# Kernel optimization log

Hardware: AMD Instinct MI355X
Metric: run time of the kernel (lower is better)

## Reference

```python
import jax, jax.numpy as jnp
import numpy as np

B, T, C, N = 2, 2048, 4096, 4096

def setup_inputs() -> dict:
    key = jax.random.key(0)
    k1, k2, k3, k4 = jax.random.split(key, 4)
    y = jax.random.normal(k1, (B, T, C), dtype=jnp.float32)
    # quantized weight: uint8 codes in [0,255], stored/used as float after upcast
    weight = jnp.round(jax.random.uniform(k2, (C, N), dtype=jnp.float32) * 255.0)
    rng = jax.random.uniform(k3, (1, 1, C), dtype=jnp.float32) * 0.01  # per-input-channel scale
    offset = jax.random.normal(k4, (C,), dtype=jnp.float32) * 0.01    # per-input-channel offset
    return {"y": y, "weight": weight, "rng": rng, "offset": offset}

def reference(y, weight, rng, offset):
    # yv = y.reshape(-1,C) @ offset -> [B,T,1] correction term
    yv = jnp.einsum('btc,c->bt', y, offset)[..., None]
    # (y * range) @ weight  (dequantized GEMM) + correction
    out = jnp.einsum('btc,cn->btn', y * rng, weight) + yv
    return out
```

## Files before the change

kernel.cpp:

```cpp
#include <hip/hip_runtime.h>

typedef unsigned short u16;
typedef unsigned int u32;
typedef unsigned char u8;
typedef signed char i8;

typedef int i32x4 __attribute__((ext_vector_type(4)));

__global__ __launch_bounds__(256) void quant_y_kernel(const float* __restrict__ y,
                                                      const float* __restrict__ rng,
                                                      const float* __restrict__ off,
                                                      uint4* __restrict__ qy,
                                                      float* __restrict__ sp,
                                                      float* __restrict__ tv) {
    const int row = blockIdx.x;
    const int tid = threadIdx.x;
    const float* yr = y + (size_t)row * 4096;
    const int base = tid * 16;

    float ysr[16];
    float amax = 0.0f, s1 = 0.0f, s2 = 0.0f;
    #pragma unroll
    for (int ii = 0; ii < 4; ++ii) {
        float4 v = *(const float4*)&yr[base + ii * 4];
        float4 g = *(const float4*)&rng[base + ii * 4];
        float4 o = *(const float4*)&off[base + ii * 4];
        float p0 = v.x * g.x, p1 = v.y * g.y, p2 = v.z * g.z, p3 = v.w * g.w;
        ysr[ii * 4 + 0] = p0; ysr[ii * 4 + 1] = p1;
        ysr[ii * 4 + 2] = p2; ysr[ii * 4 + 3] = p3;
        s1 += p0 + p1 + p2 + p3;
        s2 += v.x * o.x + v.y * o.y + v.z * o.z + v.w * o.w;
        amax = fmaxf(amax, fmaxf(fmaxf(fabsf(p0), fabsf(p1)), fmaxf(fabsf(p2), fabsf(p3))));
    }
    #pragma unroll
    for (int d = 32; d > 0; d >>= 1) {
        amax = fmaxf(amax, __shfl_down(amax, d));
        s1 += __shfl_down(s1, d);
        s2 += __shfl_down(s2, d);
    }
    __shared__ float ra[4], rs1[4], rs2[4];
    const int wv = tid >> 6;
    if ((tid & 63) == 0) { ra[wv] = amax; rs1[wv] = s1; rs2[wv] = s2; }
    __syncthreads();
    const float sm = fmaxf(fmaxf(ra[0], ra[1]), fmaxf(ra[2], ra[3]));
    const float inv = sm > 0.0f ? 127.0f / sm : 0.0f;

    u32 d[4];
    #pragma unroll
    for (int g = 0; g < 4; ++g) {
        u32 b0 = (u8)(i8)(int)rintf(ysr[g * 4 + 0] * inv);
        u32 b1 = (u8)(i8)(int)rintf(ysr[g * 4 + 1] * inv);
        u32 b2 = (u8)(i8)(int)rintf(ysr[g * 4 + 2] * inv);
        u32 b3 = (u8)(i8)(int)rintf(ysr[g * 4 + 3] * inv);
        d[g] = b0 | (b1 << 8) | (b2 << 16) | (b3 << 24);
    }
    const int j = (tid & 7) ^ (row & 7);
    qy[(size_t)row * 256 + (tid >> 3) * 8 + j] = make_uint4(d[0], d[1], d[2], d[3]);
    if (tid == 0) {
        sp[row] = sm / 127.0f;
        tv[row] = 128.0f * (rs1[0] + rs1[1] + rs1[2] + rs1[3])
                        + (rs2[0] + rs2[1] + rs2[2] + rs2[3]);
    }
}

__global__ __launch_bounds__(256) void quant_w_kernel(const float* __restrict__ w,
                                                      uint4* __restrict__ wq) {
    __shared__ i8 tile[64][68];
    const int n0 = (blockIdx.x & 63) * 64;
    const int k0 = (blockIdx.x >> 6) * 64;
    const int c4 = threadIdx.x & 15;
    const int r0 = threadIdx.x >> 4;
    #pragma unroll
    for (int i = 0; i < 4; ++i) {
        int kk = r0 + i * 16;
        float4 v = *(const float4*)&w[(size_t)(k0 + kk) * 4096 + n0 + c4 * 4];
        u32 b0 = (u8)(i8)((int)v.x - 128);
        u32 b1 = (u8)(i8)((int)v.y - 128);
        u32 b2 = (u8)(i8)((int)v.z - 128);
        u32 b3 = (u8)(i8)((int)v.w - 128);
        *(u32*)&tile[kk][c4 * 4] = b0 | (b1 << 8) | (b2 << 16) | (b3 << 24);
    }
    __syncthreads();
    const int nl = threadIdx.x >> 2;
    const int ci = threadIdx.x & 3;
    const int l = ((k0 >> 4) & 7) + ci;
    const int j = l ^ ((n0 + nl) & 7);
    u32 d[4];
    #pragma unroll
    for (int g = 0; g < 4; ++g) {
        int kl = ci * 16 + g * 4;
        d[g] = (u32)(u8)tile[kl + 0][nl] | ((u32)(u8)tile[kl + 1][nl] << 8)
             | ((u32)(u8)tile[kl + 2][nl] << 16) | ((u32)(u8)tile[kl + 3][nl] << 24);
    }
    wq[(size_t)(n0 + nl) * 256 + (k0 >> 7) * 8 + j] = make_uint4(d[0], d[1], d[2], d[3]);
}

__device__ inline void gld16(const i8* g, i8* l) {
    __builtin_amdgcn_global_load_lds((const __attribute__((address_space(1))) void*)g,
                                     (__attribute__((address_space(3))) void*)l,
                                     16, 0, 0);
}

__global__ __launch_bounds__(256) void gemm_kernel(const i8* __restrict__ qy,
                                                   const i8* __restrict__ wq,
                                                   const float* __restrict__ sp,
                                                   const float* __restrict__ tv,
                                                   float* __restrict__ out) {
    __shared__ i8 As[128 * 128];
    __shared__ i8 Bs[128 * 128];
    const int bid = blockIdx.x;
    const int xcd = bid & 7;
    const int jj = bid >> 3;
    const int bn = (xcd * 4 + (jj & 3)) * 128;
    const int bm = (jj >> 2) * 128;

    const int lane = threadIdx.x & 63;
    const int wv = threadIdx.x >> 6;
    const int wm = (wv >> 1) * 64;
    const int wn = (wv & 1) * 64;
    const int r = lane & 15;
    const int q = lane >> 4;
    const int j0 = q ^ (r & 7);

    const int rsub = lane >> 3;
    const int jsub = lane & 7;
    const i8* gA[4]; const i8* gB[4]; i8* lA[4]; i8* lB[4];
    #pragma unroll
    for (int c = 0; c < 4; ++c) {
        int ca = wv * 4 + c;
        gA[c] = qy + (size_t)(bm + ca * 8 + rsub) * 4096 + jsub * 16;
        gB[c] = wq + (size_t)(bn + ca * 8 + rsub) * 4096 + jsub * 16;
        lA[c] = &As[ca * 1024];
        lB[c] = &Bs[ca * 1024];
    }

    i32x4 acc[4][4] = {};

    for (int kt = 0; kt < 32; ++kt) {
        #pragma unroll
        for (int c = 0; c < 4; ++c) {
            gld16(gA[c], lA[c]);
            gld16(gB[c], lB[c]);
            gA[c] += 128; gB[c] += 128;
        }
        __syncthreads();

        #pragma unroll
        for (int s = 0; s < 2; ++s) {
            const int js = (j0 ^ (s * 4)) * 16;
            i32x4 af[4], bfr[4];
            #pragma unroll
            for (int i = 0; i < 4; ++i)
                af[i] = *(const i32x4*)&As[(wm + i * 16 + r) * 128 + js];
            #pragma unroll
            for (int i = 0; i < 4; ++i)
                bfr[i] = *(const i32x4*)&Bs[(wn + i * 16 + r) * 128 + js];
            #pragma unroll
            for (int i = 0; i < 4; ++i) {
                #pragma unroll
                for (int j = 0; j < 4; ++j)
                    acc[i][j] = __builtin_amdgcn_mfma_i32_16x16x64_i8(af[i], bfr[j], acc[i][j], 0, 0, 0);
            }
        }
        __syncthreads();
    }

    #pragma unroll
    for (int i = 0; i < 4; ++i) {
        #pragma unroll
        for (int rr = 0; rr < 4; ++rr) {
            const int gm = bm + wm + i * 16 + q * 4 + rr;
            const float sc = sp[gm];
            const float tt = tv[gm];
            #pragma unroll
            for (int j = 0; j < 4; ++j) {
                const int gn = bn + wn + j * 16 + r;
                out[(size_t)gm * 4096 + gn] = sc * (float)acc[i][j][rr] + tt;
            }
        }
    }
}

extern "C" void kernel_launch(void* const* d_in, const int* in_sizes, int n_in,
                              void* d_out, int out_size, void* d_ws, size_t ws_size,
                              hipStream_t stream) {
    const float* y   = (const float*)d_in[0];
    const float* w   = (const float*)d_in[1];
    const float* rng = (const float*)d_in[2];
    const float* off = (const float*)d_in[3];
    float* out = (float*)d_out;

    i8* qy = (i8*)d_ws;
    i8* wq = qy + (size_t)4096 * 4096;
    float* sp = (float*)(wq + (size_t)4096 * 4096);
    float* tv = sp + 4096;

    quant_y_kernel<<<4096, 256, 0, stream>>>(y, rng, off, (uint4*)qy, sp, tv);
    quant_w_kernel<<<4096, 256, 0, stream>>>(w, (uint4*)wq);
    gemm_kernel<<<1024, 256, 0, stream>>>(qy, wq, sp, tv, out);
}
```

Before: 244.4 us.

## Merge quantization kernels and enlarge GEMM tile to 256x128

The two quantization kernels become one launch, with block index ranges choosing between activation and weight work, which removes one kernel launch and lets the two overlap. The int8 GEMM block tile grows from 128x128 to 256x128, so each wave computes 128x64 with 32 accumulators and reuses each B fragment across eight A fragments. This halves the grid to 512 blocks and raises arithmetic intensity per LDS byte. The cost is more LDS per block (48KB) and more accumulator registers, which lowers occupancy and leaves fewer blocks to fill the CUs.

```diff
diff --git a/kernel.cpp b/kernel.cpp
--- a/kernel.cpp
+++ b/kernel.cpp
@@ -7,92 +7,92 @@
 
 typedef int i32x4 __attribute__((ext_vector_type(4)));
 
-__global__ __launch_bounds__(256) void quant_y_kernel(const float* __restrict__ y,
-                                                      const float* __restrict__ rng,
-                                                      const float* __restrict__ off,
-                                                      uint4* __restrict__ qy,
-                                                      float* __restrict__ sp,
-                                                      float* __restrict__ tv) {
-    const int row = blockIdx.x;
+__global__ __launch_bounds__(256) void prep_kernel(const float* __restrict__ y,
+                                                   const float* __restrict__ w,
+                                                   const float* __restrict__ rng,
+                                                   const float* __restrict__ off,
+                                                   uint4* __restrict__ qy,
+                                                   uint4* __restrict__ wq,
+                                                   float* __restrict__ sp,
+                                                   float* __restrict__ tv) {
     const int tid = threadIdx.x;
-    const float* yr = y + (size_t)row * 4096;
-    const int base = tid * 16;
-
-    float ysr[16];
-    float amax = 0.0f, s1 = 0.0f, s2 = 0.0f;
-    #pragma unroll
-    for (int ii = 0; ii < 4; ++ii) {
-        float4 v = *(const float4*)&yr[base + ii * 4];
-        float4 g = *(const float4*)&rng[base + ii * 4];
-        float4 o = *(const float4*)&off[base + ii * 4];
-        float p0 = v.x * g.x, p1 = v.y * g.y, p2 = v.z * g.z, p3 = v.w * g.w;
-        ysr[ii * 4 + 0] = p0; ysr[ii * 4 + 1] = p1;
-        ysr[ii * 4 + 2] = p2; ysr[ii * 4 + 3] = p3;
-        s1 += p0 + p1 + p2 + p3;
-        s2 += v.x * o.x + v.y * o.y + v.z * o.z + v.w * o.w;
-        amax = fmaxf(amax, fmaxf(fmaxf(fabsf(p0), fabsf(p1)), fmaxf(fabsf(p2), fabsf(p3))));
+    if (blockIdx.x < 4096) {
+        const int row = blockIdx.x;
+        const float* yr = y + (size_t)row * 4096;
+        const int base = tid * 16;
+        float ysr[16];
+        float amax = 0.0f, s1 = 0.0f, s2 = 0.0f;
+        #pragma unroll
+        for (int ii = 0; ii < 4; ++ii) {
+            float4 v = *(const float4*)&yr[base + ii * 4];
+            float4 g = *(const float4*)&rng[base + ii * 4];
+            float4 o = *(const float4*)&off[base + ii * 4];
+            float p0 = v.x * g.x, p1 = v.y * g.y, p2 = v.z * g.z, p3 = v.w * g.w;
+            ysr[ii * 4 + 0] = p0; ysr[ii * 4 + 1] = p1;
+            ysr[ii * 4 + 2] = p2; ysr[ii * 4 + 3] = p3;
+            s1 += p0 + p1 + p2 + p3;
+            s2 += v.x * o.x + v.y * o.y + v.z * o.z + v.w * o.w;
+            amax = fmaxf(amax, fmaxf(fmaxf(fabsf(p0), fabsf(p1)), fmaxf(fabsf(p2), fabsf(p3))));
+        }
+        #pragma unroll
+        for (int d = 32; d > 0; d >>= 1) {
+            amax = fmaxf(amax, __shfl_down(amax, d));
+            s1 += __shfl_down(s1, d);
+            s2 += __shfl_down(s2, d);
+        }
+        __shared__ float ra[4], rs1[4], rs2[4];
+        const int wv = tid >> 6;
+        if ((tid & 63) == 0) { ra[wv] = amax; rs1[wv] = s1; rs2[wv] = s2; }
+        __syncthreads();
+        const float sm = fmaxf(fmaxf(ra[0], ra[1]), fmaxf(ra[2], ra[3]));
+        const float inv = sm > 0.0f ? 127.0f / sm : 0.0f;
+        u32 d[4];
+        #pragma unroll
+        for (int g = 0; g < 4; ++g) {
+            u32 b0 = (u8)(i8)(int)rintf(ysr[g * 4 + 0] * inv);
+            u32 b1 = (u8)(i8)(int)rintf(ysr[g * 4 + 1] * inv);
+            u32 b2 = (u8)(i8)(int)rintf(ysr[g * 4 + 2] * inv);
+            u32 b3 = (u8)(i8)(int)rintf(ysr[g * 4 + 3] * inv);
+            d[g] = b0 | (b1 << 8) | (b2 << 16) | (b3 << 24);
+        }
+        const int j = (tid & 7) ^ (row & 7);
+        qy[(size_t)row * 256 + (tid >> 3) * 8 + j] = make_uint4(d[0], d[1], d[2], d[3]);
+        if (tid == 0) {
+            sp[row] = sm / 127.0f;
+            tv[row] = 128.0f * (rs1[0] + rs1[1] + rs1[2] + rs1[3])
+                            + (rs2[0] + rs2[1] + rs2[2] + rs2[3]);
+        }
+    } else {
+        __shared__ i8 tile[64][68];
+        const int b = blockIdx.x - 4096;
+        const int n0 = (b & 63) * 64;
+        const int k0 = (b >> 6) * 64;
+        const int c4 = tid & 15;
+        const int r0 = tid >> 4;
+        #pragma unroll
+        for (int i = 0; i < 4; ++i) {
+            int kk = r0 + i * 16;
+            float4 v = *(const float4*)&w[(size_t)(k0 + kk) * 4096 + n0 + c4 * 4];
+            u32 b0 = (u8)(i8)((int)v.x - 128);
+            u32 b1 = (u8)(i8)((int)v.y - 128);
+            u32 b2 = (u8)(i8)((int)v.z - 128);
+            u32 b3 = (u8)(i8)((int)v.w - 128);
+            *(u32*)&tile[kk][c4 * 4] = b0 | (b1 << 8) | (b2 << 16) | (b3 << 24);
+        }
+        __syncthreads();
+        const int nl = tid >> 2;
+        const int ci = tid & 3;
+        const int l = ((k0 >> 4) & 7) + ci;
+        const int j = l ^ ((n0 + nl) & 7);
+        u32 d[4];
+        #pragma unroll
+        for (int g = 0; g < 4; ++g) {
+            int kl = ci * 16 + g * 4;
+            d[g] = (u32)(u8)tile[kl + 0][nl] | ((u32)(u8)tile[kl + 1][nl] << 8)
+                 | ((u32)(u8)tile[kl + 2][nl] << 16) | ((u32)(u8)tile[kl + 3][nl] << 24);
+        }
+        wq[(size_t)(n0 + nl) * 256 + (k0 >> 7) * 8 + j] = make_uint4(d[0], d[1], d[2], d[3]);
     }
-    #pragma unroll
-    for (int d = 32; d > 0; d >>= 1) {
-        amax = fmaxf(amax, __shfl_down(amax, d));
-        s1 += __shfl_down(s1, d);
-        s2 += __shfl_down(s2, d);
-    }
-    __shared__ float ra[4], rs1[4], rs2[4];
-    const int wv = tid >> 6;
-    if ((tid & 63) == 0) { ra[wv] = amax; rs1[wv] = s1; rs2[wv] = s2; }
-    __syncthreads();
-    const float sm = fmaxf(fmaxf(ra[0], ra[1]), fmaxf(ra[2], ra[3]));
-    const float inv = sm > 0.0f ? 127.0f / sm : 0.0f;
-
-    u32 d[4];
-    #pragma unroll
-    for (int g = 0; g < 4; ++g) {
-        u32 b0 = (u8)(i8)(int)rintf(ysr[g * 4 + 0] * inv);
-        u32 b1 = (u8)(i8)(int)rintf(ysr[g * 4 + 1] * inv);
-        u32 b2 = (u8)(i8)(int)rintf(ysr[g * 4 + 2] * inv);
-        u32 b3 = (u8)(i8)(int)rintf(ysr[g * 4 + 3] * inv);
-        d[g] = b0 | (b1 << 8) | (b2 << 16) | (b3 << 24);
-    }
-    const int j = (tid & 7) ^ (row & 7);
-    qy[(size_t)row * 256 + (tid >> 3) * 8 + j] = make_uint4(d[0], d[1], d[2], d[3]);
-    if (tid == 0) {
-        sp[row] = sm / 127.0f;
-        tv[row] = 128.0f * (rs1[0] + rs1[1] + rs1[2] + rs1[3])
-                        + (rs2[0] + rs2[1] + rs2[2] + rs2[3]);
-    }
-}
-
-__global__ __launch_bounds__(256) void quant_w_kernel(const float* __restrict__ w,
-                                                      uint4* __restrict__ wq) {
-    __shared__ i8 tile[64][68];
-    const int n0 = (blockIdx.x & 63) * 64;
-    const int k0 = (blockIdx.x >> 6) * 64;
-    const int c4 = threadIdx.x & 15;
-    const int r0 = threadIdx.x >> 4;
-    #pragma unroll
-    for (int i = 0; i < 4; ++i) {
-        int kk = r0 + i * 16;
-        float4 v = *(const float4*)&w[(size_t)(k0 + kk) * 4096 + n0 + c4 * 4];
-        u32 b0 = (u8)(i8)((int)v.x - 128);
-        u32 b1 = (u8)(i8)((int)v.y - 128);
-        u32 b2 = (u8)(i8)((int)v.z - 128);
-        u32 b3 = (u8)(i8)((int)v.w - 128);
-        *(u32*)&tile[kk][c4 * 4] = b0 | (b1 << 8) | (b2 << 16) | (b3 << 24);
-    }
-    __syncthreads();
-    const int nl = threadIdx.x >> 2;
-    const int ci = threadIdx.x & 3;
-    const int l = ((k0 >> 4) & 7) + ci;
-    const int j = l ^ ((n0 + nl) & 7);
-    u32 d[4];
-    #pragma unroll
-    for (int g = 0; g < 4; ++g) {
-        int kl = ci * 16 + g * 4;
-        d[g] = (u32)(u8)tile[kl + 0][nl] | ((u32)(u8)tile[kl + 1][nl] << 8)
-             | ((u32)(u8)tile[kl + 2][nl] << 16) | ((u32)(u8)tile[kl + 3][nl] << 24);
-    }
-    wq[(size_t)(n0 + nl) * 256 + (k0 >> 7) * 8 + j] = make_uint4(d[0], d[1], d[2], d[3]);
 }
 
 __device__ inline void gld16(const i8* g, i8* l) {
@@ -106,17 +106,17 @@
                                                    const float* __restrict__ sp,
                                                    const float* __restrict__ tv,
                                                    float* __restrict__ out) {
-    __shared__ i8 As[128 * 128];
+    __shared__ i8 As[256 * 128];
     __shared__ i8 Bs[128 * 128];
     const int bid = blockIdx.x;
     const int xcd = bid & 7;
     const int jj = bid >> 3;
     const int bn = (xcd * 4 + (jj & 3)) * 128;
-    const int bm = (jj >> 2) * 128;
+    const int bm = (jj >> 2) * 256;
 
     const int lane = threadIdx.x & 63;
     const int wv = threadIdx.x >> 6;
-    const int wm = (wv >> 1) * 64;
+    const int wm = (wv >> 1) * 128;
     const int wn = (wv & 1) * 64;
     const int r = lane & 15;
     const int q = lane >> 4;
@@ -124,49 +124,43 @@
 
     const int rsub = lane >> 3;
     const int jsub = lane & 7;
-    const i8* gA[4]; const i8* gB[4]; i8* lA[4]; i8* lB[4];
-    #pragma unroll
-    for (int c = 0; c < 4; ++c) {
-        int ca = wv * 4 + c;
-        gA[c] = qy + (size_t)(bm + ca * 8 + rsub) * 4096 + jsub * 16;
-        gB[c] = wq + (size_t)(bn + ca * 8 + rsub) * 4096 + jsub * 16;
-        lA[c] = &As[ca * 1024];
-        lB[c] = &Bs[ca * 1024];
-    }
+    const i8* vA = qy + (size_t)(bm + wv * 64 + rsub) * 4096 + jsub * 16;
+    const i8* vB = wq + (size_t)(bn + wv * 32 + rsub) * 4096 + jsub * 16;
+    i8* lA = &As[wv * 8 * 1024 + lane * 16];
+    i8* lB = &Bs[wv * 4 * 1024 + lane * 16];
 
-    i32x4 acc[4][4] = {};
+    i32x4 acc[8][4] = {};
 
     for (int kt = 0; kt < 32; ++kt) {
+        const int koff = kt * 128;
         #pragma unroll
-        for (int c = 0; c < 4; ++c) {
-            gld16(gA[c], lA[c]);
-            gld16(gB[c], lB[c]);
-            gA[c] += 128; gB[c] += 128;
-        }
+        for (int c = 0; c < 8; ++c)
+            gld16(vA + (size_t)c * 32768 + koff, lA + c * 1024);
+        #pragma unroll
+        for (int c = 0; c < 4; ++c)
+            gld16(vB + (size_t)c * 32768 + koff, lB + c * 1024);
         __syncthreads();
 
         #pragma unroll
         for (int s = 0; s < 2; ++s) {
             const int js = (j0 ^ (s * 4)) * 16;
-            i32x4 af[4], bfr[4];
+            i32x4 bfr[4];
             #pragma unroll
-            for (int i = 0; i < 4; ++i)
-                af[i] = *(const i32x4*)&As[(wm + i * 16 + r) * 128 + js];
+            for (int j = 0; j < 4; ++j)
+                bfr[j] = *(const i32x4*)&Bs[(wn + j * 16 + r) * 128 + js];
             #pragma unroll
-            for (int i = 0; i < 4; ++i)
-                bfr[i] = *(const i32x4*)&Bs[(wn + i * 16 + r) * 128 + js];
-            #pragma unroll
-            for (int i = 0; i < 4; ++i) {
+            for (int i = 0; i < 8; ++i) {
+                i32x4 af = *(const i32x4*)&As[(wm + i * 16 + r) * 128 + js];
                 #pragma unroll
                 for (int j = 0; j < 4; ++j)
-                    acc[i][j] = __builtin_amdgcn_mfma_i32_16x16x64_i8(af[i], bfr[j], acc[i][j], 0, 0, 0);
+                    acc[i][j] = __builtin_amdgcn_mfma_i32_16x16x64_i8(af, bfr[j], acc[i][j], 0, 0, 0);
             }
         }
         __syncthreads();
     }
 
     #pragma unroll
-    for (int i = 0; i < 4; ++i) {
+    for (int i = 0; i < 8; ++i) {
         #pragma unroll
         for (int rr = 0; rr < 4; ++rr) {
             const int gm = bm + wm + i * 16 + q * 4 + rr;
@@ -195,7 +189,6 @@
     float* sp = (float*)(wq + (size_t)4096 * 4096);
     float* tv = sp + 4096;
 
-    quant_y_kernel<<<4096, 256, 0, stream>>>(y, rng, off, (uint4*)qy, sp, tv);
-    quant_w_kernel<<<4096, 256, 0, stream>>>(w, (uint4*)wq);
-    gemm_kernel<<<1024, 256, 0, stream>>>(qy, wq, sp, tv, out);
+    prep_kernel<<<8192, 256, 0, stream>>>(y, w, rng, off, (uint4*)qy, (uint4*)wq, sp, tv);
+    gemm_kernel<<<512, 256, 0, stream>>>(qy, wq, sp, tv, out);
 }
```

After: 280.8 us. 1.15x slower.
